# Optimization experiments

Measured on AMD Instinct MI355X. Metric: run time of the kernel, lower is better.

## Reference

```python
import jax, jax.numpy as jnp
import numpy as np

N, T, F_IN = 20000, 8, 64
FILTERS, HEADS = 32, 4
E = 320000
LEAKY = 0.2  # PyG GATConv default negative_slope
HID = HEADS * FILTERS  # 128


def setup_inputs() -> dict:
    key = jax.random.key(0)
    ks = jax.random.split(key, 16)
    g = lambda k, shape, scale: jax.random.normal(k, shape, dtype=jnp.float32) * scale
    return {
        "x": g(ks[0], (N, T, F_IN), 1.0),
        "edge_index": jax.random.randint(ks[1], (2, E), 0, N, dtype=jnp.int32),
        # GATConv 1: lin weight, attention vectors (per head), bias
        "W1": g(ks[2], (HID, F_IN), (2.0 / F_IN) ** 0.5),
        "att_src1": g(ks[3], (HEADS, FILTERS), 0.1),
        "att_dst1": g(ks[4], (HEADS, FILTERS), 0.1),
        "b1": jnp.zeros((HID,), jnp.float32),
        # GATConv 2
        "W2": g(ks[5], (HID, HID), (2.0 / HID) ** 0.5),
        "att_src2": g(ks[6], (HEADS, FILTERS), 0.1),
        "att_dst2": g(ks[7], (HEADS, FILTERS), 0.1),
        "b2": jnp.zeros((HID,), jnp.float32),
        # MLP head
        "lw1": g(ks[8], (FILTERS, HID), (2.0 / HID) ** 0.5),
        "lb1": jnp.zeros((FILTERS,), jnp.float32),
        "lw2": g(ks[9], (1, FILTERS), (2.0 / FILTERS) ** 0.5),
        "lb2": jnp.zeros((1,), jnp.float32),
    }


def gat_layer(x, src, dst, W, a_src, a_dst, b):
    """PyG GATConv (concat=True, add_self_loops already applied to src/dst)."""
    h = (x @ W.T).reshape(N, HEADS, FILTERS)          # [N,H,F]
    es = (h * a_src).sum(-1)                          # [N,H] per-node src score
    ed = (h * a_dst).sum(-1)                          # [N,H] per-node dst score
    e = jax.nn.leaky_relu(es[src] + ed[dst], LEAKY)   # [E',H]
    # segment softmax over incoming edges per destination node
    m = jax.ops.segment_max(e, dst, num_segments=N)
    ex = jnp.exp(e - m[dst])
    denom = jax.ops.segment_sum(ex, dst, num_segments=N)
    alpha = ex / (denom[dst] + 1e-16)                 # [E',H]
    out = jax.ops.segment_sum(h[src] * alpha[:, :, None], dst, num_segments=N)
    return out.reshape(N, HID) + b


def reference(x, edge_index, W1, att_src1, att_dst1, b1,
              W2, att_src2, att_dst2, b2, lw1, lb1, lw2, lb2):
    # add self loops (PyG GATConv default add_self_loops=True)
    loop = jnp.arange(N, dtype=edge_index.dtype)
    src = jnp.concatenate([edge_index[0], loop])
    dst = jnp.concatenate([edge_index[1], loop])

    def step(_, x_t):
        h = jax.nn.elu(gat_layer(x_t, src, dst, W1, att_src1, att_dst1, b1))
        # dropout is identity in eval mode
        h = jax.nn.elu(gat_layer(h, src, dst, W2, att_src2, att_dst2, b2))
        h = jax.nn.relu(h @ lw1.T + lb1)
        y = h @ lw2.T + lb2                            # [N,1]
        return None, y

    _, ys = jax.lax.scan(step, None, jnp.transpose(x, (1, 0, 2)))  # scan over T
    return ys  # [T, N, 1] (stacked version of the original list of outputs)
```

## Files before the change

kernel.cpp:

```cpp
#include <hip/hip_runtime.h>

constexpr int cN     = 20000;
constexpr int cT     = 8;
constexpr int cFIN   = 64;
constexpr int cHEADS = 4;
constexpr int cF     = 32;
constexpr int cHID   = 128;
constexpr int cE     = 320000;
constexpr int cET    = cE + cN;
constexpr int cR     = cN * cT;
constexpr float cLEAKY = 0.2f;
constexpr float cL2E = 1.44269504088896340736f;

typedef __attribute__((ext_vector_type(8))) short bf16x8;
typedef __attribute__((ext_vector_type(4))) float f32x4;

static __device__ __forceinline__ unsigned short f2bfu(float f) {
    unsigned int u;
    __builtin_memcpy(&u, &f, 4);
    u += 0x7FFFu + ((u >> 16) & 1u);
    return (unsigned short)(u >> 16);
}
static __device__ __forceinline__ void unpack2(unsigned int v, float& lo, float& hi) {
    unsigned int ul = v << 16, uh = v & 0xFFFF0000u;
    __builtin_memcpy(&lo, &ul, 4);
    __builtin_memcpy(&hi, &uh, 4);
}
static __device__ __forceinline__ unsigned int pack2(float lo, float hi) {
    unsigned int ul, uh;
    __builtin_memcpy(&ul, &lo, 4);
    __builtin_memcpy(&uh, &hi, 4);
    ul += 0x7FFFu + ((ul >> 16) & 1u);
    uh += 0x7FFFu + ((uh >> 16) & 1u);
    return (ul >> 16) | (uh & 0xFFFF0000u);
}

__global__ void cvt_w_kernel(const float* W1, const float* W2, const float* lw1,
                             unsigned short* W1b, unsigned short* W2b, unsigned short* lw1b) {
    int i = blockIdx.x * 256 + threadIdx.x;
    if (i < cHID * cFIN)                      W1b[i] = f2bfu(W1[i]);
    else if (i < cHID * cFIN + cHID * cHID)   W2b[i - cHID * cFIN] = f2bfu(W2[i - cHID * cFIN]);
    else if (i < cHID * cFIN + cHID * cHID + cF * cHID)
        lw1b[i - cHID * cFIN - cHID * cHID] = f2bfu(lw1[i - cHID * cFIN - cHID * cHID]);
}

__global__ void deg_init_kernel(int* deg) {
    int n = blockIdx.x * blockDim.x + threadIdx.x;
    if (n < cN) deg[n] = 1;
}
__global__ void deg_count_kernel(const int* ei, int* deg) {
    int e = blockIdx.x * blockDim.x + threadIdx.x;
    if (e < cE) atomicAdd(&deg[ei[cE + e]], 1);
}
__global__ void scan_kernel(const int* deg, int* offs, int* cur) {
    __shared__ int sdeg[79 * 256];
    __shared__ int lds[256];
    int tid = threadIdx.x;
    #pragma unroll 4
    for (int k = 0; k < 79; k++) {
        int idx = k * 256 + tid;
        sdeg[idx] = (idx < cN) ? deg[idx] : 0;
    }
    __syncthreads();
    const int CH = 79;
    int base = tid * CH;
    int tot = 0;
    #pragma unroll 8
    for (int j = 0; j < CH; j++) tot += sdeg[base + j];
    lds[tid] = tot;
    __syncthreads();
    for (int off = 1; off < 256; off <<= 1) {
        int v = (tid >= off) ? lds[tid - off] : 0;
        __syncthreads();
        lds[tid] += v;
        __syncthreads();
    }
    int run = lds[tid] - tot;
    for (int j = 0; j < CH; j++) {
        int idx = base + j;
        if (idx < cN) { offs[idx] = run; cur[idx] = run; run += sdeg[idx]; }
    }
    if (tid == 255) offs[cN] = lds[255];
}
__global__ void scatter_kernel(const int* ei, int* cur, int* csr) {
    int e = blockIdx.x * blockDim.x + threadIdx.x;
    if (e >= cET) return;
    int s, d;
    if (e < cE) { s = ei[e]; d = ei[cE + e]; }
    else        { s = e - cE; d = s; }
    int pos = atomicAdd(&cur[d], 1);
    csr[pos] = s;
}

__global__ __launch_bounds__(256) void gemm1_fused_kernel(
        const float* __restrict__ x, const unsigned short* __restrict__ W,
        const float* __restrict__ a_src, const float* __restrict__ a_dst,
        unsigned short* __restrict__ hb, float* __restrict__ es, float* __restrict__ ed) {
    __shared__ float hl[64][132];
    int tid  = threadIdx.x;
    int wave = tid >> 6;
    int lane = tid & 63;
    int q    = lane >> 4;
    int mi   = lane & 15;
    int m0   = blockIdx.x * 64 + wave * 16;

    int rho = m0 + mi;
    int t = rho / cN;
    int n = rho - t * cN;
    const float* xr = x + (size_t)n * (cT * cFIN) + t * cFIN;

    bf16x8 afrag[2];
    #pragma unroll
    for (int s = 0; s < 2; s++) {
        float4 v0 = *(const float4*)(xr + s * 32 + q * 8);
        float4 v1 = *(const float4*)(xr + s * 32 + q * 8 + 4);
        bf16x8 f;
        f[0] = (short)f2bfu(v0.x); f[1] = (short)f2bfu(v0.y);
        f[2] = (short)f2bfu(v0.z); f[3] = (short)f2bfu(v0.w);
        f[4] = (short)f2bfu(v1.x); f[5] = (short)f2bfu(v1.y);
        f[6] = (short)f2bfu(v1.z); f[7] = (short)f2bfu(v1.w);
        afrag[s] = f;
    }

    f32x4 acc[8];
    #pragma unroll
    for (int ct = 0; ct < 8; ct++) acc[ct] = (f32x4){0.f, 0.f, 0.f, 0.f};
    #pragma unroll
    for (int ct = 0; ct < 8; ct++) {
        int c = ct * 16 + mi;
        #pragma unroll
        for (int s = 0; s < 2; s++) {
            bf16x8 bfrag = *(const bf16x8*)(W + (size_t)c * cFIN + s * 32 + q * 8);
            acc[ct] = __builtin_amdgcn_mfma_f32_16x16x32_bf16(afrag[s], bfrag, acc[ct], 0, 0, 0);
        }
    }

    #pragma unroll
    for (int ct = 0; ct < 8; ct++)
        #pragma unroll
        for (int r = 0; r < 4; r++)
            hl[wave * 16 + q * 4 + r][ct * 16 + mi] = acc[ct][r];
    __syncthreads();

    {
        int r2 = tid & 63;
        int hd = tid >> 6;
        int rg = blockIdx.x * 64 + r2;
        const float* hr = &hl[r2][hd * cF];
        const float* sa = a_src + hd * cF;
        const float* da = a_dst + hd * cF;
        float s1 = 0.f, s2 = 0.f;
        #pragma unroll 8
        for (int f = 0; f < cF; f++) {
            float hv = hr[f];
            s1 += hv * sa[f];
            s2 += hv * da[f];
        }
        es[rg * cHEADS + hd] = s1 * cL2E;
        ed[rg * cHEADS + hd] = s2 * cL2E;
    }

    size_t base = (size_t)blockIdx.x * 64 * cHID;
    #pragma unroll
    for (int it = 0; it < 8; it++) {
        int g   = tid + it * 256;
        int row = g >> 5;
        int c4  = (g & 31) * 4;
        float4 v = *(const float4*)&hl[row][c4];
        unsigned int p0 = pack2(v.x, v.y), p1 = pack2(v.z, v.w);
        *(uint2*)(hb + base + (size_t)row * cHID + c4) = make_uint2(p0, p1);
    }
}

static __device__ __forceinline__ void agg_core(
        const unsigned short* __restrict__ hb, const float* __restrict__ es,
        const float* __restrict__ ed, const int* __restrict__ offs,
        const int* __restrict__ csr, const float* __restrict__ bias,
        int t, int n, int j, float* r) {
    int head = j >> 2;
    int rho  = t * cN + n;
    int s0 = offs[n], s1 = offs[n + 1];
    float edn = ed[(size_t)rho * cHEADS + head];
    const char* hpc = (const char*)(hb + (size_t)t * cN * cHID);
    const char* epc = (const char*)(es + (size_t)t * cN * cHEADS);
    const char* cc  = (const char*)csr;
    unsigned jo = (unsigned)j * 16u;
    unsigned ho = (unsigned)head * 4u;

    float acc[8] = {};
    float den = 0.f;
    int i = s0;
    for (; i + 3 < s1; i += 4) {
        unsigned io = (unsigned)i * 4u;
        int sa = *(const int*)(cc + io);
        int sb = *(const int*)(cc + io + 4u);
        int sc = *(const int*)(cc + io + 8u);
        int sd = *(const int*)(cc + io + 12u);
        uint4 ra = *(const uint4*)(hpc + (((unsigned)sa) << 8) + jo);
        uint4 rb = *(const uint4*)(hpc + (((unsigned)sb) << 8) + jo);
        uint4 rc = *(const uint4*)(hpc + (((unsigned)sc) << 8) + jo);
        uint4 rd = *(const uint4*)(hpc + (((unsigned)sd) << 8) + jo);
        float ea = *(const float*)(epc + (((unsigned)sa) << 4) + ho) + edn;
        float eb = *(const float*)(epc + (((unsigned)sb) << 4) + ho) + edn;
        float ec = *(const float*)(epc + (((unsigned)sc) << 4) + ho) + edn;
        float ee = *(const float*)(epc + (((unsigned)sd) << 4) + ho) + edn;
        ea = (ea >= 0.f) ? ea : cLEAKY * ea;
        eb = (eb >= 0.f) ? eb : cLEAKY * eb;
        ec = (ec >= 0.f) ? ec : cLEAKY * ec;
        ee = (ee >= 0.f) ? ee : cLEAKY * ee;
        float wa = __builtin_amdgcn_exp2f(ea), wb = __builtin_amdgcn_exp2f(eb);
        float wc = __builtin_amdgcn_exp2f(ec), wd = __builtin_amdgcn_exp2f(ee);
        den += wa; den += wb; den += wc; den += wd;
        float lo, hi;
        unpack2(ra.x, lo, hi); acc[0] += wa * lo; acc[1] += wa * hi;
        unpack2(ra.y, lo, hi); acc[2] += wa * lo; acc[3] += wa * hi;
        unpack2(ra.z, lo, hi); acc[4] += wa * lo; acc[5] += wa * hi;
        unpack2(ra.w, lo, hi); acc[6] += wa * lo; acc[7] += wa * hi;
        unpack2(rb.x, lo, hi); acc[0] += wb * lo; acc[1] += wb * hi;
        unpack2(rb.y, lo, hi); acc[2] += wb * lo; acc[3] += wb * hi;
        unpack2(rb.z, lo, hi); acc[4] += wb * lo; acc[5] += wb * hi;
        unpack2(rb.w, lo, hi); acc[6] += wb * lo; acc[7] += wb * hi;
        unpack2(rc.x, lo, hi); acc[0] += wc * lo; acc[1] += wc * hi;
        unpack2(rc.y, lo, hi); acc[2] += wc * lo; acc[3] += wc * hi;
        unpack2(rc.z, lo, hi); acc[4] += wc * lo; acc[5] += wc * hi;
        unpack2(rc.w, lo, hi); acc[6] += wc * lo; acc[7] += wc * hi;
        unpack2(rd.x, lo, hi); acc[0] += wd * lo; acc[1] += wd * hi;
        unpack2(rd.y, lo, hi); acc[2] += wd * lo; acc[3] += wd * hi;
        unpack2(rd.z, lo, hi); acc[4] += wd * lo; acc[5] += wd * hi;
        unpack2(rd.w, lo, hi); acc[6] += wd * lo; acc[7] += wd * hi;
    }
    for (; i < s1; i++) {
        int sa = *(const int*)(cc + (unsigned)i * 4u);
        uint4 ra = *(const uint4*)(hpc + (((unsigned)sa) << 8) + jo);
        float ea = *(const float*)(epc + (((unsigned)sa) << 4) + ho) + edn;
        ea = (ea >= 0.f) ? ea : cLEAKY * ea;
        float wa = __builtin_amdgcn_exp2f(ea);
        den += wa;
        float lo, hi;
        unpack2(ra.x, lo, hi); acc[0] += wa * lo; acc[1] += wa * hi;
        unpack2(ra.y, lo, hi); acc[2] += wa * lo; acc[3] += wa * hi;
        unpack2(ra.z, lo, hi); acc[4] += wa * lo; acc[5] += wa * hi;
        unpack2(ra.w, lo, hi); acc[6] += wa * lo; acc[7] += wa * hi;
    }
    float inv = 1.f / (den + 1e-16f);
    float4 b0 = *(const float4*)(bias + 8 * j);
    float4 b1v = *(const float4*)(bias + 8 * j + 4);
    float v0 = acc[0] * inv + b0.x;  r[0] = (v0 > 0.f) ? v0 : expm1f(v0);
    float v1 = acc[1] * inv + b0.y;  r[1] = (v1 > 0.f) ? v1 : expm1f(v1);
    float v2 = acc[2] * inv + b0.z;  r[2] = (v2 > 0.f) ? v2 : expm1f(v2);
    float v3 = acc[3] * inv + b0.w;  r[3] = (v3 > 0.f) ? v3 : expm1f(v3);
    float v4 = acc[4] * inv + b1v.x; r[4] = (v4 > 0.f) ? v4 : expm1f(v4);
    float v5 = acc[5] * inv + b1v.y; r[5] = (v5 > 0.f) ? v5 : expm1f(v5);
    float v6 = acc[6] * inv + b1v.z; r[6] = (v6 > 0.f) ? v6 : expm1f(v6);
    float v7 = acc[7] * inv + b1v.w; r[7] = (v7 > 0.f) ? v7 : expm1f(v7);
}

__global__ __launch_bounds__(256) void agg_gemm_kernel(
        const unsigned short* __restrict__ hb, const float* __restrict__ es,
        const float* __restrict__ ed, const int* __restrict__ offs,
        const int* __restrict__ csr, const float* __restrict__ bias,
        const unsigned short* __restrict__ W2, const float* __restrict__ a_src,
        const float* __restrict__ a_dst, unsigned short* __restrict__ hb2,
        float* __restrict__ es2, float* __restrict__ ed2) {
    __shared__ unsigned short tile[16 * 128];
    __shared__ float hl[16][132];
    int b    = blockIdx.x;
    int t    = b & 7;
    int g    = b >> 3;
    int tid  = threadIdx.x;
    int lrow = tid >> 4;
    int j    = tid & 15;
    int n0   = g * 16;

    float r[8];
    agg_core(hb, es, ed, offs, csr, bias, t, n0 + lrow, j, r);
    {
        uint4 o;
        o.x = pack2(r[0], r[1]); o.y = pack2(r[2], r[3]);
        o.z = pack2(r[4], r[5]); o.w = pack2(r[6], r[7]);
        unsigned tb = (unsigned)lrow * 256u + (((unsigned)j * 16u) ^ (((unsigned)(lrow & 7)) << 4));
        *(uint4*)((char*)tile + tb) = o;
    }
    __syncthreads();

    int wave = tid >> 6;
    int lane = tid & 63;
    int q    = lane >> 4;
    int mi   = lane & 15;
    bf16x8 afrag[4];
    #pragma unroll
    for (int s = 0; s < 4; s++) {
        unsigned addr = (unsigned)mi * 256u +
                        (((unsigned)(s * 64 + q * 16)) ^ (((unsigned)(mi & 7)) << 4));
        afrag[s] = *(const bf16x8*)((const char*)tile + addr);
    }
    f32x4 acc2[2];
    acc2[0] = (f32x4){0.f, 0.f, 0.f, 0.f};
    acc2[1] = (f32x4){0.f, 0.f, 0.f, 0.f};
    #pragma unroll
    for (int ct = 0; ct < 2; ct++) {
        int c = (wave * 2 + ct) * 16 + mi;
        #pragma unroll
        for (int s = 0; s < 4; s++) {
            bf16x8 bfrag = *(const bf16x8*)(W2 + (size_t)c * cHID + s * 32 + q * 8);
            acc2[ct] = __builtin_amdgcn_mfma_f32_16x16x32_bf16(afrag[s], bfrag, acc2[ct], 0, 0, 0);
        }
    }
    #pragma unroll
    for (int ct = 0; ct < 2; ct++)
        #pragma unroll
        for (int rr = 0; rr < 4; rr++)
            hl[q * 4 + rr][(wave * 2 + ct) * 16 + mi] = acc2[ct][rr];
    __syncthreads();

    if (tid < 64) {
        int r2 = tid & 15;
        int hd = tid >> 4;
        int rg = t * cN + n0 + r2;
        const float* hr = &hl[r2][hd * cF];
        const float* sa = a_src + hd * cF;
        const float* da = a_dst + hd * cF;
        float s1 = 0.f, s2 = 0.f;
        #pragma unroll 8
        for (int f = 0; f < cF; f++) {
            float hv = hr[f];
            s1 += hv * sa[f];
            s2 += hv * da[f];
        }
        es2[(size_t)rg * cHEADS + hd] = s1 * cL2E;
        ed2[(size_t)rg * cHEADS + hd] = s2 * cL2E;
    }
    {
        int row = tid >> 4;
        int c8  = (tid & 15) * 8;
        float4 v0 = *(const float4*)&hl[row][c8];
        float4 v1 = *(const float4*)&hl[row][c8 + 4];
        uint4 o;
        o.x = pack2(v0.x, v0.y); o.y = pack2(v0.z, v0.w);
        o.z = pack2(v1.x, v1.y); o.w = pack2(v1.z, v1.w);
        *(uint4*)(hb2 + (size_t)(t * cN + n0 + row) * cHID + c8) = o;
    }
}

__global__ __launch_bounds__(256) void TemporalGAT_20005957665499_kernel(
        const unsigned short* __restrict__ hb2, const float* __restrict__ es,
        const float* __restrict__ ed, const int* __restrict__ offs,
        const int* __restrict__ csr, const float* __restrict__ bias,
        const unsigned short* __restrict__ lw1b, const float* __restrict__ lb1,
        const float* __restrict__ lw2, const float* __restrict__ lb2,
        float* __restrict__ out) {
    __shared__ unsigned short tile[16 * 128];
    int b    = blockIdx.x;
    int t    = b & 7;
    int g    = b >> 3;
    int tid  = threadIdx.x;
    int lrow = tid >> 4;
    int j    = tid & 15;
    int n0   = g * 16;

    float r[8];
    agg_core(hb2, es, ed, offs, csr, bias, t, n0 + lrow, j, r);
    {
        uint4 o;
        o.x = pack2(r[0], r[1]); o.y = pack2(r[2], r[3]);
        o.z = pack2(r[4], r[5]); o.w = pack2(r[6], r[7]);
        unsigned tb = (unsigned)lrow * 256u + (((unsigned)j * 16u) ^ (((unsigned)(lrow & 7)) << 4));
        *(uint4*)((char*)tile + tb) = o;
    }
    __syncthreads();

    if (tid < 64) {
        int q  = tid >> 4;
        int mi = tid & 15;
        bf16x8 afrag[4];
        #pragma unroll
        for (int s = 0; s < 4; s++) {
            unsigned addr = (unsigned)mi * 256u +
                            (((unsigned)(s * 64 + q * 16)) ^ (((unsigned)(mi & 7)) << 4));
            afrag[s] = *(const bf16x8*)((const char*)tile + addr);
        }
        f32x4 acc2[2];
        acc2[0] = (f32x4){0.f, 0.f, 0.f, 0.f};
        acc2[1] = (f32x4){0.f, 0.f, 0.f, 0.f};
        #pragma unroll
        for (int ct = 0; ct < 2; ct++) {
            int c = ct * 16 + mi;
            #pragma unroll
            for (int s = 0; s < 4; s++) {
                bf16x8 bfrag = *(const bf16x8*)(lw1b + (size_t)c * cHID + s * 32 + q * 8);
                acc2[ct] = __builtin_amdgcn_mfma_f32_16x16x32_bf16(afrag[s], bfrag, acc2[ct], 0, 0, 0);
            }
        }
        float lb1a = lb1[mi], lb1b_ = lb1[16 + mi];
        float lw2a = lw2[mi], lw2b_ = lw2[16 + mi];
        float l2 = lb2[0];
        #pragma unroll
        for (int rr = 0; rr < 4; rr++) {
            float va = fmaxf(acc2[0][rr] + lb1a, 0.f);
            float vb = fmaxf(acc2[1][rr] + lb1b_, 0.f);
            float v = va * lw2a + vb * lw2b_;
            v += __shfl_xor(v, 1);
            v += __shfl_xor(v, 2);
            v += __shfl_xor(v, 4);
            v += __shfl_xor(v, 8);
            if (mi == 0) out[t * cN + n0 + q * 4 + rr] = v + l2;
        }
    }
}

extern "C" void kernel_launch(void* const* d_in, const int* in_sizes, int n_in,
                              void* d_out, int out_size, void* d_ws, size_t ws_size,
                              hipStream_t stream) {
    const float* x   = (const float*)d_in[0];
    const int*   ei  = (const int*)d_in[1];
    const float* W1  = (const float*)d_in[2];
    const float* as1 = (const float*)d_in[3];
    const float* ad1 = (const float*)d_in[4];
    const float* b1  = (const float*)d_in[5];
    const float* W2  = (const float*)d_in[6];
    const float* as2 = (const float*)d_in[7];
    const float* ad2 = (const float*)d_in[8];
    const float* b2  = (const float*)d_in[9];
    const float* lw1 = (const float*)d_in[10];
    const float* lb1 = (const float*)d_in[11];
    const float* lw2 = (const float*)d_in[12];
    const float* lb2 = (const float*)d_in[13];
    float* out = (float*)d_out;
    (void)in_sizes; (void)n_in; (void)out_size; (void)ws_size;

    char* ws = (char*)d_ws;
    size_t o = 0;
    auto carveN = [&](size_t bytes) { void* p = ws + o; o += (bytes + 255) & ~(size_t)255; return p; };
    unsigned short* hb   = (unsigned short*)carveN((size_t)cR * cHID * 2);
    unsigned short* hb2  = (unsigned short*)carveN((size_t)cR * cHID * 2);
    unsigned short* W1b  = (unsigned short*)carveN((size_t)cHID * cFIN * 2);
    unsigned short* W2b  = (unsigned short*)carveN((size_t)cHID * cHID * 2);
    unsigned short* lw1b = (unsigned short*)carveN((size_t)cF * cHID * 2);
    float* es1_buf = (float*)carveN((size_t)cR * cHEADS * 4);
    float* ed1_buf = (float*)carveN((size_t)cR * cHEADS * 4);
    float* es2_buf = (float*)carveN((size_t)cR * cHEADS * 4);
    float* ed2_buf = (float*)carveN((size_t)cR * cHEADS * 4);
    int*   deg     = (int*)carveN((size_t)cN * 4);
    int*   offs    = (int*)carveN((size_t)(cN + 1) * 4);
    int*   cursor  = (int*)carveN((size_t)cN * 4);
    int*   csr     = (int*)carveN((size_t)cET * 4);

    cvt_w_kernel<<<(cHID * cFIN + cHID * cHID + cF * cHID + 255) / 256, 256, 0, stream>>>(
        W1, W2, lw1, W1b, W2b, lw1b);

    deg_init_kernel<<<(cN + 255) / 256, 256, 0, stream>>>(deg);
    deg_count_kernel<<<(cE + 255) / 256, 256, 0, stream>>>(ei, deg);
    scan_kernel<<<1, 256, 0, stream>>>(deg, offs, cursor);
    scatter_kernel<<<(cET + 255) / 256, 256, 0, stream>>>(ei, cursor, csr);

    gemm1_fused_kernel<<<cR / 64, 256, 0, stream>>>(x, W1b, as1, ad1, hb, es1_buf, ed1_buf);
    agg_gemm_kernel<<<(cN / 16) * cT, 256, 0, stream>>>(
        hb, es1_buf, ed1_buf, offs, csr, b1, W2b, as2, ad2, hb2, es2_buf, ed2_buf);
    TemporalGAT_20005957665499_kernel<<<(cN / 16) * cT, 256, 0, stream>>>(
        hb2, es2_buf, ed2_buf, offs, csr, b2, lw1b, lb1, lw2, lb2, out);
}
```

Before: 382.8 us.

## Sort nodes by in-degree so each aggregation block handles similar-degree rows

Builds a degree-bucketed permutation of nodes inside the single-block scan kernel, using a shared-memory histogram and counting sort. The two aggregation kernels then process permuted nodes, so the 16 rows in a block have similar edge counts. This is meant to cut load imbalance, where threads wait on the highest-degree row in their block. In exchange, the scan kernel does extra serial work, and reads and writes become scattered rather than contiguous in node order.

```diff
diff --git a/kernel.cpp b/kernel.cpp
--- a/kernel.cpp
+++ b/kernel.cpp
@@ -52,15 +52,17 @@
     int e = blockIdx.x * blockDim.x + threadIdx.x;
     if (e < cE) atomicAdd(&deg[ei[cE + e]], 1);
 }
-__global__ void scan_kernel(const int* deg, int* offs, int* cur) {
+__global__ void scan_kernel(const int* deg, int* offs, int* cur, int* perm) {
     __shared__ int sdeg[79 * 256];
     __shared__ int lds[256];
+    __shared__ int hbin[64];
     int tid = threadIdx.x;
     #pragma unroll 4
     for (int k = 0; k < 79; k++) {
         int idx = k * 256 + tid;
         sdeg[idx] = (idx < cN) ? deg[idx] : 0;
     }
+    if (tid < 64) hbin[tid] = 0;
     __syncthreads();
     const int CH = 79;
     int base = tid * CH;
@@ -68,6 +70,10 @@
     #pragma unroll 8
     for (int j = 0; j < CH; j++) tot += sdeg[base + j];
     lds[tid] = tot;
+    for (int j = 0; j < CH; j++) {
+        int idx = base + j;
+        if (idx < cN) atomicAdd(&hbin[min(sdeg[idx], 63)], 1);
+    }
     __syncthreads();
     for (int off = 1; off < 256; off <<= 1) {
         int v = (tid >= off) ? lds[tid - off] : 0;
@@ -81,6 +87,19 @@
         if (idx < cN) { offs[idx] = run; cur[idx] = run; run += sdeg[idx]; }
     }
     if (tid == 255) offs[cN] = lds[255];
+    __syncthreads();
+    if (tid == 0) {
+        int r2 = 0;
+        for (int b = 0; b < 64; b++) { int c = hbin[b]; hbin[b] = r2; r2 += c; }
+    }
+    __syncthreads();
+    for (int j = 0; j < CH; j++) {
+        int idx = base + j;
+        if (idx < cN) {
+            int pos = atomicAdd(&hbin[min(sdeg[idx], 63)], 1);
+            perm[pos] = idx;
+        }
+    }
 }
 __global__ void scatter_kernel(const int* ei, int* cur, int* csr) {
     int e = blockIdx.x * blockDim.x + threadIdx.x;
@@ -258,12 +277,14 @@
 __global__ __launch_bounds__(256) void agg_gemm_kernel(
         const unsigned short* __restrict__ hb, const float* __restrict__ es,
         const float* __restrict__ ed, const int* __restrict__ offs,
-        const int* __restrict__ csr, const float* __restrict__ bias,
+        const int* __restrict__ csr, const int* __restrict__ perm,
+        const float* __restrict__ bias,
         const unsigned short* __restrict__ W2, const float* __restrict__ a_src,
         const float* __restrict__ a_dst, unsigned short* __restrict__ hb2,
         float* __restrict__ es2, float* __restrict__ ed2) {
     __shared__ unsigned short tile[16 * 128];
     __shared__ float hl[16][132];
+    __shared__ int nodes[16];
     int b    = blockIdx.x;
     int t    = b & 7;
     int g    = b >> 3;
@@ -272,8 +293,12 @@
     int j    = tid & 15;
     int n0   = g * 16;
 
+    if (tid < 16) nodes[tid] = perm[n0 + tid];
+    __syncthreads();
+    int n = nodes[lrow];
+
     float r[8];
-    agg_core(hb, es, ed, offs, csr, bias, t, n0 + lrow, j, r);
+    agg_core(hb, es, ed, offs, csr, bias, t, n, j, r);
     {
         uint4 o;
         o.x = pack2(r[0], r[1]); o.y = pack2(r[2], r[3]);
@@ -316,7 +341,7 @@
     if (tid < 64) {
         int r2 = tid & 15;
         int hd = tid >> 4;
-        int rg = t * cN + n0 + r2;
+        int rg = t * cN + nodes[r2];
         const float* hr = &hl[r2][hd * cF];
         const float* sa = a_src + hd * cF;
         const float* da = a_dst + hd * cF;
@@ -338,18 +363,20 @@
         uint4 o;
         o.x = pack2(v0.x, v0.y); o.y = pack2(v0.z, v0.w);
         o.z = pack2(v1.x, v1.y); o.w = pack2(v1.z, v1.w);
-        *(uint4*)(hb2 + (size_t)(t * cN + n0 + row) * cHID + c8) = o;
+        *(uint4*)(hb2 + (size_t)(t * cN + nodes[row]) * cHID + c8) = o;
     }
 }
 
 __global__ __launch_bounds__(256) void TemporalGAT_20005957665499_kernel(
         const unsigned short* __restrict__ hb2, const float* __restrict__ es,
         const float* __restrict__ ed, const int* __restrict__ offs,
-        const int* __restrict__ csr, const float* __restrict__ bias,
+        const int* __restrict__ csr, const int* __restrict__ perm,
+        const float* __restrict__ bias,
         const unsigned short* __restrict__ lw1b, const float* __restrict__ lb1,
         const float* __restrict__ lw2, const float* __restrict__ lb2,
         float* __restrict__ out) {
     __shared__ unsigned short tile[16 * 128];
+    __shared__ int nodes[16];
     int b    = blockIdx.x;
     int t    = b & 7;
     int g    = b >> 3;
@@ -358,8 +385,12 @@
     int j    = tid & 15;
     int n0   = g * 16;
 
+    if (tid < 16) nodes[tid] = perm[n0 + tid];
+    __syncthreads();
+    int n = nodes[lrow];
+
     float r[8];
-    agg_core(hb2, es, ed, offs, csr, bias, t, n0 + lrow, j, r);
+    agg_core(hb2, es, ed, offs, csr, bias, t, n, j, r);
     {
         uint4 o;
         o.x = pack2(r[0], r[1]); o.y = pack2(r[2], r[3]);
@@ -403,7 +434,7 @@
             v += __shfl_xor(v, 2);
             v += __shfl_xor(v, 4);
             v += __shfl_xor(v, 8);
-            if (mi == 0) out[t * cN + n0 + q * 4 + rr] = v + l2;
+            if (mi == 0) out[t * cN + nodes[q * 4 + rr]] = v + l2;
         }
     }
 }
@@ -444,18 +475,19 @@
     int*   offs    = (int*)carveN((size_t)(cN + 1) * 4);
     int*   cursor  = (int*)carveN((size_t)cN * 4);
     int*   csr     = (int*)carveN((size_t)cET * 4);
+    int*   perm    = (int*)carveN((size_t)cN * 4);
 
     cvt_w_kernel<<<(cHID * cFIN + cHID * cHID + cF * cHID + 255) / 256, 256, 0, stream>>>(
         W1, W2, lw1, W1b, W2b, lw1b);
 
     deg_init_kernel<<<(cN + 255) / 256, 256, 0, stream>>>(deg);
     deg_count_kernel<<<(cE + 255) / 256, 256, 0, stream>>>(ei, deg);
-    scan_kernel<<<1, 256, 0, stream>>>(deg, offs, cursor);
+    scan_kernel<<<1, 256, 0, stream>>>(deg, offs, cursor, perm);
     scatter_kernel<<<(cET + 255) / 256, 256, 0, stream>>>(ei, cursor, csr);
 
     gemm1_fused_kernel<<<cR / 64, 256, 0, stream>>>(x, W1b, as1, ad1, hb, es1_buf, ed1_buf);
     agg_gemm_kernel<<<(cN / 16) * cT, 256, 0, stream>>>(
-        hb, es1_buf, ed1_buf, offs, csr, b1, W2b, as2, ad2, hb2, es2_buf, ed2_buf);
+        hb, es1_buf, ed1_buf, offs, csr, perm, b1, W2b, as2, ad2, hb2, es2_buf, ed2_buf);
     TemporalGAT_20005957665499_kernel<<<(cN / 16) * cT, 256, 0, stream>>>(
-        hb2, es2_buf, ed2_buf, offs, csr, b2, lw1b, lb1, lw2, lb2, out);
-}
+        hb2, es2_buf, ed2_buf, offs, csr, perm, b2, lw1b, lb1, lw2, lb2, out);
+}
```

Measured after the change: 389.1 us. About the same (+1.6%).

## Process two timesteps per aggregation block and merge degree-count with weight conversion

Applied to the files above, without the earlier changes.

The two aggregation kernels now give each block two timesteps (t and t+4) for the same 16 destination nodes. The CSR neighbour indices and offsets are then read once and reused across both timesteps, and twice as many independent gathers are in flight per thread. The grid halves, while register pressure and shared memory per block roughly double. Separately, the degree-init and degree-count kernels are folded into the weight conversion kernel with a memset, and the self-loop +1 moves into the scan, which removes a launch.

```diff
diff --git a/kernel.cpp b/kernel.cpp
--- a/kernel.cpp
+++ b/kernel.cpp
@@ -34,24 +34,40 @@
     uh += 0x7FFFu + ((uh >> 16) & 1u);
     return (ul >> 16) | (uh & 0xFFFF0000u);
 }
-
-__global__ void cvt_w_kernel(const float* W1, const float* W2, const float* lw1,
-                             unsigned short* W1b, unsigned short* W2b, unsigned short* lw1b) {
+static __device__ __forceinline__ void fma8(uint4 r, float w, float* acc) {
+    float lo, hi;
+    unpack2(r.x, lo, hi); acc[0] += w * lo; acc[1] += w * hi;
+    unpack2(r.y, lo, hi); acc[2] += w * lo; acc[3] += w * hi;
+    unpack2(r.z, lo, hi); acc[4] += w * lo; acc[5] += w * hi;
+    unpack2(r.w, lo, hi); acc[6] += w * lo; acc[7] += w * hi;
+}
+static __device__ __forceinline__ void finish8(const float* acc, float den,
+                                               const float* bias, int j, float* r) {
+    float inv = 1.f / (den + 1e-16f);
+    float4 b0 = *(const float4*)(bias + 8 * j);
+    float4 b1 = *(const float4*)(bias + 8 * j + 4);
+    float v;
+    v = acc[0] * inv + b0.x; r[0] = (v > 0.f) ? v : expm1f(v);
+    v = acc[1] * inv + b0.y; r[1] = (v > 0.f) ? v : expm1f(v);
+    v = acc[2] * inv + b0.z; r[2] = (v > 0.f) ? v : expm1f(v);
+    v = acc[3] * inv + b0.w; r[3] = (v > 0.f) ? v : expm1f(v);
+    v = acc[4] * inv + b1.x; r[4] = (v > 0.f) ? v : expm1f(v);
+    v = acc[5] * inv + b1.y; r[5] = (v > 0.f) ? v : expm1f(v);
+    v = acc[6] * inv + b1.z; r[6] = (v > 0.f) ? v : expm1f(v);
+    v = acc[7] * inv + b1.w; r[7] = (v > 0.f) ? v : expm1f(v);
+}
+
+__global__ void cvt_deg_kernel(const float* W1, const float* W2, const float* lw1,
+                               const int* ei, unsigned short* W1b, unsigned short* W2b,
+                               unsigned short* lw1b, int* deg) {
     int i = blockIdx.x * 256 + threadIdx.x;
     if (i < cHID * cFIN)                      W1b[i] = f2bfu(W1[i]);
     else if (i < cHID * cFIN + cHID * cHID)   W2b[i - cHID * cFIN] = f2bfu(W2[i - cHID * cFIN]);
     else if (i < cHID * cFIN + cHID * cHID + cF * cHID)
         lw1b[i - cHID * cFIN - cHID * cHID] = f2bfu(lw1[i - cHID * cFIN - cHID * cHID]);
-}
-
-__global__ void deg_init_kernel(int* deg) {
-    int n = blockIdx.x * blockDim.x + threadIdx.x;
-    if (n < cN) deg[n] = 1;
-}
-__global__ void deg_count_kernel(const int* ei, int* deg) {
-    int e = blockIdx.x * blockDim.x + threadIdx.x;
-    if (e < cE) atomicAdd(&deg[ei[cE + e]], 1);
-}
+    if (i < cE) atomicAdd(&deg[ei[cE + i]], 1);
+}
+
 __global__ void scan_kernel(const int* deg, int* offs, int* cur) {
     __shared__ int sdeg[79 * 256];
     __shared__ int lds[256];
@@ -59,7 +75,7 @@
     #pragma unroll 4
     for (int k = 0; k < 79; k++) {
         int idx = k * 256 + tid;
-        sdeg[idx] = (idx < cN) ? deg[idx] : 0;
+        sdeg[idx] = (idx < cN) ? deg[idx] + 1 : 0;
     }
     __syncthreads();
     const int CH = 79;
@@ -172,23 +188,25 @@
     }
 }
 
-static __device__ __forceinline__ void agg_core(
+static __device__ __forceinline__ void agg_core2(
         const unsigned short* __restrict__ hb, const float* __restrict__ es,
         const float* __restrict__ ed, const int* __restrict__ offs,
         const int* __restrict__ csr, const float* __restrict__ bias,
-        int t, int n, int j, float* r) {
+        int tA, int tB, int n, int j, float* rA, float* rB) {
     int head = j >> 2;
-    int rho  = t * cN + n;
     int s0 = offs[n], s1 = offs[n + 1];
-    float edn = ed[(size_t)rho * cHEADS + head];
-    const char* hpc = (const char*)(hb + (size_t)t * cN * cHID);
-    const char* epc = (const char*)(es + (size_t)t * cN * cHEADS);
+    float ednA = ed[(size_t)(tA * cN + n) * cHEADS + head];
+    float ednB = ed[(size_t)(tB * cN + n) * cHEADS + head];
+    const char* hpA = (const char*)(hb + (size_t)tA * cN * cHID);
+    const char* hpB = (const char*)(hb + (size_t)tB * cN * cHID);
+    const char* epA = (const char*)(es + (size_t)tA * cN * cHEADS);
+    const char* epB = (const char*)(es + (size_t)tB * cN * cHEADS);
     const char* cc  = (const char*)csr;
     unsigned jo = (unsigned)j * 16u;
     unsigned ho = (unsigned)head * 4u;
 
-    float acc[8] = {};
-    float den = 0.f;
+    float accA[8] = {}, accB[8] = {};
+    float denA = 0.f, denB = 0.f;
     int i = s0;
     for (; i + 3 < s1; i += 4) {
         unsigned io = (unsigned)i * 4u;
@@ -196,63 +214,63 @@
         int sb = *(const int*)(cc + io + 4u);
         int sc = *(const int*)(cc + io + 8u);
         int sd = *(const int*)(cc + io + 12u);
-        uint4 ra = *(const uint4*)(hpc + (((unsigned)sa) << 8) + jo);
-        uint4 rb = *(const uint4*)(hpc + (((unsigned)sb) << 8) + jo);
-        uint4 rc = *(const uint4*)(hpc + (((unsigned)sc) << 8) + jo);
-        uint4 rd = *(const uint4*)(hpc + (((unsigned)sd) << 8) + jo);
-        float ea = *(const float*)(epc + (((unsigned)sa) << 4) + ho) + edn;
-        float eb = *(const float*)(epc + (((unsigned)sb) << 4) + ho) + edn;
-        float ec = *(const float*)(epc + (((unsigned)sc) << 4) + ho) + edn;
-        float ee = *(const float*)(epc + (((unsigned)sd) << 4) + ho) + edn;
-        ea = (ea >= 0.f) ? ea : cLEAKY * ea;
-        eb = (eb >= 0.f) ? eb : cLEAKY * eb;
-        ec = (ec >= 0.f) ? ec : cLEAKY * ec;
-        ee = (ee >= 0.f) ? ee : cLEAKY * ee;
-        float wa = __builtin_amdgcn_exp2f(ea), wb = __builtin_amdgcn_exp2f(eb);
-        float wc = __builtin_amdgcn_exp2f(ec), wd = __builtin_amdgcn_exp2f(ee);
-        den += wa; den += wb; den += wc; den += wd;
-        float lo, hi;
-        unpack2(ra.x, lo, hi); acc[0] += wa * lo; acc[1] += wa * hi;
-        unpack2(ra.y, lo, hi); acc[2] += wa * lo; acc[3] += wa * hi;
-        unpack2(ra.z, lo, hi); acc[4] += wa * lo; acc[5] += wa * hi;
-        unpack2(ra.w, lo, hi); acc[6] += wa * lo; acc[7] += wa * hi;
-        unpack2(rb.x, lo, hi); acc[0] += wb * lo; acc[1] += wb * hi;
-        unpack2(rb.y, lo, hi); acc[2] += wb * lo; acc[3] += wb * hi;
-        unpack2(rb.z, lo, hi); acc[4] += wb * lo; acc[5] += wb * hi;
-        unpack2(rb.w, lo, hi); acc[6] += wb * lo; acc[7] += wb * hi;
-        unpack2(rc.x, lo, hi); acc[0] += wc * lo; acc[1] += wc * hi;
-        unpack2(rc.y, lo, hi); acc[2] += wc * lo; acc[3] += wc * hi;
-        unpack2(rc.z, lo, hi); acc[4] += wc * lo; acc[5] += wc * hi;
-        unpack2(rc.w, lo, hi); acc[6] += wc * lo; acc[7] += wc * hi;
-        unpack2(rd.x, lo, hi); acc[0] += wd * lo; acc[1] += wd * hi;
-        unpack2(rd.y, lo, hi); acc[2] += wd * lo; acc[3] += wd * hi;
-        unpack2(rd.z, lo, hi); acc[4] += wd * lo; acc[5] += wd * hi;
-        unpack2(rd.w, lo, hi); acc[6] += wd * lo; acc[7] += wd * hi;
+        unsigned oa = ((unsigned)sa) << 8, ob = ((unsigned)sb) << 8;
+        unsigned oc = ((unsigned)sc) << 8, od = ((unsigned)sd) << 8;
+        uint4 raA = *(const uint4*)(hpA + oa + jo);
+        uint4 rbA = *(const uint4*)(hpA + ob + jo);
+        uint4 rcA = *(const uint4*)(hpA + oc + jo);
+        uint4 rdA = *(const uint4*)(hpA + od + jo);
+        uint4 raB = *(const uint4*)(hpB + oa + jo);
+        uint4 rbB = *(const uint4*)(hpB + ob + jo);
+        uint4 rcB = *(const uint4*)(hpB + oc + jo);
+        uint4 rdB = *(const uint4*)(hpB + od + jo);
+        unsigned ea4 = (((unsigned)sa) << 4) + ho, eb4 = (((unsigned)sb) << 4) + ho;
+        unsigned ec4 = (((unsigned)sc) << 4) + ho, ed4 = (((unsigned)sd) << 4) + ho;
+        float eaA = *(const float*)(epA + ea4) + ednA;
+        float ebA = *(const float*)(epA + eb4) + ednA;
+        float ecA = *(const float*)(epA + ec4) + ednA;
+        float eeA = *(const float*)(epA + ed4) + ednA;
+        float eaB = *(const float*)(epB + ea4) + ednB;
+        float ebB = *(const float*)(epB + eb4) + ednB;
+        float ecB = *(const float*)(epB + ec4) + ednB;
+        float eeB = *(const float*)(epB + ed4) + ednB;
+        eaA = (eaA >= 0.f) ? eaA : cLEAKY * eaA;
+        ebA = (ebA >= 0.f) ? ebA : cLEAKY * ebA;
+        ecA = (ecA >= 0.f) ? ecA : cLEAKY * ecA;
+        eeA = (eeA >= 0.f) ? eeA : cLEAKY * eeA;
+        eaB = (eaB >= 0.f) ? eaB : cLEAKY * eaB;
+        ebB = (ebB >= 0.f) ? ebB : cLEAKY * ebB;
+        ecB = (ecB >= 0.f) ? ecB : cLEAKY * ecB;
+        eeB = (eeB >= 0.f) ? eeB : cLEAKY * eeB;
+        float waA = __builtin_amdgcn_exp2f(eaA), wbA = __builtin_amdgcn_exp2f(ebA);
+        float wcA = __builtin_amdgcn_exp2f(ecA), wdA = __builtin_amdgcn_exp2f(eeA);
+        float waB = __builtin_amdgcn_exp2f(eaB), wbB = __builtin_amdgcn_exp2f(ebB);
+        float wcB = __builtin_amdgcn_exp2f(ecB), wdB = __builtin_amdgcn_exp2f(eeB);
+        denA += waA; denA += wbA; denA += wcA; denA += wdA;
+        denB += waB; denB += wbB; denB += wcB; denB += wdB;
+        fma8(raA, waA, accA); fma8(rbA, wbA, accA);
+        fma8(rcA, wcA, accA); fma8(rdA, wdA, accA);
+        fma8(raB, waB, accB); fma8(rbB, wbB, accB);
+        fma8(rcB, wcB, accB); fma8(rdB, wdB, accB);
     }
     for (; i < s1; i++) {
         int sa = *(const int*)(cc + (unsigned)i * 4u);
-        uint4 ra = *(const uint4*)(hpc + (((unsigned)sa) << 8) + jo);
-        float ea = *(const float*)(epc + (((unsigned)sa) << 4) + ho) + edn;
-        ea = (ea >= 0.f) ? ea : cLEAKY * ea;
-        float wa = __builtin_amdgcn_exp2f(ea);
-        den += wa;
-        float lo, hi;
-        unpack2(ra.x, lo, hi); acc[0] += wa * lo; acc[1] += wa * hi;
-        unpack2(ra.y, lo, hi); acc[2] += wa * lo; acc[3] += wa * hi;
-        unpack2(ra.z, lo, hi); acc[4] += wa * lo; acc[5] += wa * hi;
-        unpack2(ra.w, lo, hi); acc[6] += wa * lo; acc[7] += wa * hi;
-    }
-    float inv = 1.f / (den + 1e-16f);
-    float4 b0 = *(const float4*)(bias + 8 * j);
-    float4 b1v = *(const float4*)(bias + 8 * j + 4);
-    float v0 = acc[0] * inv + b0.x;  r[0] = (v0 > 0.f) ? v0 : expm1f(v0);
-    float v1 = acc[1] * inv + b0.y;  r[1] = (v1 > 0.f) ? v1 : expm1f(v1);
-    float v2 = acc[2] * inv + b0.z;  r[2] = (v2 > 0.f) ? v2 : expm1f(v2);
-    float v3 = acc[3] * inv + b0.w;  r[3] = (v3 > 0.f) ? v3 : expm1f(v3);
-    float v4 = acc[4] * inv + b1v.x; r[4] = (v4 > 0.f) ? v4 : expm1f(v4);
-    float v5 = acc[5] * inv + b1v.y; r[5] = (v5 > 0.f) ? v5 : expm1f(v5);
-    float v6 = acc[6] * inv + b1v.z; r[6] = (v6 > 0.f) ? v6 : expm1f(v6);
-    float v7 = acc[7] * inv + b1v.w; r[7] = (v7 > 0.f) ? v7 : expm1f(v7);
+        unsigned oa = ((unsigned)sa) << 8;
+        unsigned ea4 = (((unsigned)sa) << 4) + ho;
+        uint4 raA = *(const uint4*)(hpA + oa + jo);
+        uint4 raB = *(const uint4*)(hpB + oa + jo);
+        float eaA = *(const float*)(epA + ea4) + ednA;
+        float eaB = *(const float*)(epB + ea4) + ednB;
+        eaA = (eaA >= 0.f) ? eaA : cLEAKY * eaA;
+        eaB = (eaB >= 0.f) ? eaB : cLEAKY * eaB;
+        float waA = __builtin_amdgcn_exp2f(eaA);
+        float waB = __builtin_amdgcn_exp2f(eaB);
+        denA += waA; denB += waB;
+        fma8(raA, waA, accA);
+        fma8(raB, waB, accB);
+    }
+    finish8(accA, denA, bias, j, rA);
+    finish8(accB, denB, bias, j, rB);
 }
 
 __global__ __launch_bounds__(256) void agg_gemm_kernel(
@@ -262,24 +280,32 @@
         const unsigned short* __restrict__ W2, const float* __restrict__ a_src,
         const float* __restrict__ a_dst, unsigned short* __restrict__ hb2,
         float* __restrict__ es2, float* __restrict__ ed2) {
-    __shared__ unsigned short tile[16 * 128];
-    __shared__ float hl[16][132];
+    __shared__ unsigned short tile[2][16 * 128];
+    __shared__ float hl[2][16][132];
     int b    = blockIdx.x;
-    int t    = b & 7;
-    int g    = b >> 3;
+    int tp   = b & 3;
+    int g    = b >> 2;
+    int tA   = tp, tB = tp + 4;
     int tid  = threadIdx.x;
     int lrow = tid >> 4;
     int j    = tid & 15;
     int n0   = g * 16;
-
-    float r[8];
-    agg_core(hb, es, ed, offs, csr, bias, t, n0 + lrow, j, r);
+    int n    = n0 + lrow;
+
+    float rA[8], rB[8];
+    agg_core2(hb, es, ed, offs, csr, bias, tA, tB, n, j, rA, rB);
+    unsigned tb = (unsigned)lrow * 256u + (((unsigned)j * 16u) ^ (((unsigned)(lrow & 7)) << 4));
     {
         uint4 o;
-        o.x = pack2(r[0], r[1]); o.y = pack2(r[2], r[3]);
-        o.z = pack2(r[4], r[5]); o.w = pack2(r[6], r[7]);
-        unsigned tb = (unsigned)lrow * 256u + (((unsigned)j * 16u) ^ (((unsigned)(lrow & 7)) << 4));
-        *(uint4*)((char*)tile + tb) = o;
+        o.x = pack2(rA[0], rA[1]); o.y = pack2(rA[2], rA[3]);
+        o.z = pack2(rA[4], rA[5]); o.w = pack2(rA[6], rA[7]);
+        *(uint4*)((char*)tile[0] + tb) = o;
+    }
+    {
+        uint4 o;
+        o.x = pack2(rB[0], rB[1]); o.y = pack2(rB[2], rB[3]);
+        o.z = pack2(rB[4], rB[5]); o.w = pack2(rB[6], rB[7]);
+        *(uint4*)((char*)tile[1] + tb) = o;
     }
     __syncthreads();
 
@@ -287,37 +313,43 @@
     int lane = tid & 63;
     int q    = lane >> 4;
     int mi   = lane & 15;
-    bf16x8 afrag[4];
+    bf16x8 afA[4], afB[4];
     #pragma unroll
     for (int s = 0; s < 4; s++) {
         unsigned addr = (unsigned)mi * 256u +
                         (((unsigned)(s * 64 + q * 16)) ^ (((unsigned)(mi & 7)) << 4));
-        afrag[s] = *(const bf16x8*)((const char*)tile + addr);
-    }
-    f32x4 acc2[2];
-    acc2[0] = (f32x4){0.f, 0.f, 0.f, 0.f};
-    acc2[1] = (f32x4){0.f, 0.f, 0.f, 0.f};
+        afA[s] = *(const bf16x8*)((const char*)tile[0] + addr);
+        afB[s] = *(const bf16x8*)((const char*)tile[1] + addr);
+    }
+    f32x4 aA[2], aB[2];
+    aA[0] = (f32x4){0.f, 0.f, 0.f, 0.f}; aA[1] = aA[0];
+    aB[0] = aA[0]; aB[1] = aA[0];
     #pragma unroll
     for (int ct = 0; ct < 2; ct++) {
         int c = (wave * 2 + ct) * 16 + mi;
         #pragma unroll
         for (int s = 0; s < 4; s++) {
             bf16x8 bfrag = *(const bf16x8*)(W2 + (size_t)c * cHID + s * 32 + q * 8);
-            acc2[ct] = __builtin_amdgcn_mfma_f32_16x16x32_bf16(afrag[s], bfrag, acc2[ct], 0, 0, 0);
+            aA[ct] = __builtin_amdgcn_mfma_f32_16x16x32_bf16(afA[s], bfrag, aA[ct], 0, 0, 0);
+            aB[ct] = __builtin_amdgcn_mfma_f32_16x16x32_bf16(afB[s], bfrag, aB[ct], 0, 0, 0);
         }
     }
     #pragma unroll
     for (int ct = 0; ct < 2; ct++)
         #pragma unroll
-        for (int rr = 0; rr < 4; rr++)
-            hl[q * 4 + rr][(wave * 2 + ct) * 16 + mi] = acc2[ct][rr];
+        for (int rr = 0; rr < 4; rr++) {
+            hl[0][q * 4 + rr][(wave * 2 + ct) * 16 + mi] = aA[ct][rr];
+            hl[1][q * 4 + rr][(wave * 2 + ct) * 16 + mi] = aB[ct][rr];
+        }
     __syncthreads();
 
-    if (tid < 64) {
+    if (tid < 128) {
+        int p  = tid >> 6;
         int r2 = tid & 15;
-        int hd = tid >> 4;
-        int rg = t * cN + n0 + r2;
-        const float* hr = &hl[r2][hd * cF];
+        int hd = (tid >> 4) & 3;
+        int tcur = p ? tB : tA;
+        int rg = tcur * cN + n0 + r2;
+        const float* hr = &hl[p][r2][hd * cF];
         const float* sa = a_src + hd * cF;
         const float* da = a_dst + hd * cF;
         float s1 = 0.f, s2 = 0.f;
@@ -330,15 +362,17 @@
         es2[(size_t)rg * cHEADS + hd] = s1 * cL2E;
         ed2[(size_t)rg * cHEADS + hd] = s2 * cL2E;
     }
-    {
+    #pragma unroll
+    for (int p = 0; p < 2; p++) {
         int row = tid >> 4;
         int c8  = (tid & 15) * 8;
-        float4 v0 = *(const float4*)&hl[row][c8];
-        float4 v1 = *(const float4*)&hl[row][c8 + 4];
+        int tcur = p ? tB : tA;
+        float4 v0 = *(const float4*)&hl[p][row][c8];
+        float4 v1 = *(const float4*)&hl[p][row][c8 + 4];
         uint4 o;
         o.x = pack2(v0.x, v0.y); o.y = pack2(v0.z, v0.w);
         o.z = pack2(v1.x, v1.y); o.w = pack2(v1.z, v1.w);
-        *(uint4*)(hb2 + (size_t)(t * cN + n0 + row) * cHID + c8) = o;
+        *(uint4*)(hb2 + (size_t)(tcur * cN + n0 + row) * cHID + c8) = o;
     }
 }
 
@@ -349,39 +383,51 @@
         const unsigned short* __restrict__ lw1b, const float* __restrict__ lb1,
         const float* __restrict__ lw2, const float* __restrict__ lb2,
         float* __restrict__ out) {
-    __shared__ unsigned short tile[16 * 128];
+    __shared__ unsigned short tile[2][16 * 128];
     int b    = blockIdx.x;
-    int t    = b & 7;
-    int g    = b >> 3;
+    int tp   = b & 3;
+    int g    = b >> 2;
+    int tA   = tp, tB = tp + 4;
     int tid  = threadIdx.x;
     int lrow = tid >> 4;
     int j    = tid & 15;
     int n0   = g * 16;
-
-    float r[8];
-    agg_core(hb2, es, ed, offs, csr, bias, t, n0 + lrow, j, r);
+    int n    = n0 + lrow;
+
+    float rA[8], rB[8];
+    agg_core2(hb2, es, ed, offs, csr, bias, tA, tB, n, j, rA, rB);
+    unsigned tb = (unsigned)lrow * 256u + (((unsigned)j * 16u) ^ (((unsigned)(lrow & 7)) << 4));
     {
         uint4 o;
-        o.x = pack2(r[0], r[1]); o.y = pack2(r[2], r[3]);
-        o.z = pack2(r[4], r[5]); o.w = pack2(r[6], r[7]);
-        unsigned tb = (unsigned)lrow * 256u + (((unsigned)j * 16u) ^ (((unsigned)(lrow & 7)) << 4));
-        *(uint4*)((char*)tile + tb) = o;
+        o.x = pack2(rA[0], rA[1]); o.y = pack2(rA[2], rA[3]);
+        o.z = pack2(rA[4], rA[5]); o.w = pack2(rA[6], rA[7]);
+        *(uint4*)((char*)tile[0] + tb) = o;
+    }
+    {
+        uint4 o;
+        o.x = pack2(rB[0], rB[1]); o.y = pack2(rB[2], rB[3]);
+        o.z = pack2(rB[4], rB[5]); o.w = pack2(rB[6], rB[7]);
+        *(uint4*)((char*)tile[1] + tb) = o;
     }
     __syncthreads();
 
-    if (tid < 64) {
-        int q  = tid >> 4;
-        int mi = tid & 15;
+    int wave = tid >> 6;
+    if (wave < 2) {
+        int p  = wave;
+        int t  = p ? tB : tA;
+        int lane = tid & 63;
+        int q  = lane >> 4;
+        int mi = lane & 15;
         bf16x8 afrag[4];
         #pragma unroll
         for (int s = 0; s < 4; s++) {
             unsigned addr = (unsigned)mi * 256u +
                             (((unsigned)(s * 64 + q * 16)) ^ (((unsigned)(mi & 7)) << 4));
-            afrag[s] = *(const bf16x8*)((const char*)tile + addr);
+            afrag[s] = *(const bf16x8*)((const char*)tile[p] + addr);
         }
         f32x4 acc2[2];
         acc2[0] = (f32x4){0.f, 0.f, 0.f, 0.f};
-        acc2[1] = (f32x4){0.f, 0.f, 0.f, 0.f};
+        acc2[1] = acc2[0];
         #pragma unroll
         for (int ct = 0; ct < 2; ct++) {
             int c = ct * 16 + mi;
@@ -445,17 +491,14 @@
     int*   cursor  = (int*)carveN((size_t)cN * 4);
     int*   csr     = (int*)carveN((size_t)cET * 4);
 
-    cvt_w_kernel<<<(cHID * cFIN + cHID * cHID + cF * cHID + 255) / 256, 256, 0, stream>>>(
-        W1, W2, lw1, W1b, W2b, lw1b);
-
-    deg_init_kernel<<<(cN + 255) / 256, 256, 0, stream>>>(deg);
-    deg_count_kernel<<<(cE + 255) / 256, 256, 0, stream>>>(ei, deg);
+    hipMemsetAsync(deg, 0, (size_t)cN * 4, stream);
+    cvt_deg_kernel<<<(cE + 255) / 256, 256, 0, stream>>>(W1, W2, lw1, ei, W1b, W2b, lw1b, deg);
     scan_kernel<<<1, 256, 0, stream>>>(deg, offs, cursor);
     scatter_kernel<<<(cET + 255) / 256, 256, 0, stream>>>(ei, cursor, csr);
 
     gemm1_fused_kernel<<<cR / 64, 256, 0, stream>>>(x, W1b, as1, ad1, hb, es1_buf, ed1_buf);
-    agg_gemm_kernel<<<(cN / 16) * cT, 256, 0, stream>>>(
+    agg_gemm_kernel<<<(cN / 16) * (cT / 2), 256, 0, stream>>>(
         hb, es1_buf, ed1_buf, offs, csr, b1, W2b, as2, ad2, hb2, es2_buf, ed2_buf);
-    TemporalGAT_20005957665499_kernel<<<(cN / 16) * cT, 256, 0, stream>>>(
+    TemporalGAT_20005957665499_kernel<<<(cN / 16) * (cT / 2), 256, 0, stream>>>(
         hb2, es2_buf, ed2_buf, offs, csr, b2, lw1b, lb1, lw2, lb2, out);
 }
```

New measurement: 437.7 us. +14.3%, slower.
